# Kernel tuning notes

Hardware: AMD Instinct MI355X
Metric: run time of the kernel (lower is better)

The kernel has to match this reference:

```python
import jax, jax.numpy as jnp
import numpy as np

# config constants (match init_kwargs)
C = 1024
NH = 16
HS = C // NH
CHUNK = 64          # attn_chunk_size
TOPK = 32           # attn_topk
WINDOW = 4096       # kv_cache_window_size
MIN_KV = 16384      # min_kv_cache_size
MAX_KV = 32768      # max_kv_cache_size
SHORT = 4096        # short_sequence_criteria
CT = 65536          # incoming kv-cache length


def setup_inputs() -> dict:
    key = jax.random.key(0)
    ks = jax.random.split(key, 7)
    s = 1.0 / np.sqrt(C)
    return {
        "x": jax.random.normal(ks[0], (C,), jnp.float32),
        "k_cache": jax.random.normal(ks[1], (1, CT, C), jnp.float32),
        "v_cache": jax.random.normal(ks[2], (1, CT, C), jnp.float32),
        "Wr": jax.random.normal(ks[3], (C, C), jnp.float32) * s,
        "Wk": jax.random.normal(ks[4], (C, C), jnp.float32) * s,
        "Wv": jax.random.normal(ks[5], (C, C), jnp.float32) * s,
        "Wo": jax.random.normal(ks[6], (C, C), jnp.float32) * s,
    }


def _split_heads(t):  # (1, T, C) -> (1, NH, T, HS)
    return t.reshape(1, t.shape[1], NH, HS).transpose(0, 2, 1, 3)


def _update_kv_cache(q, k_cache, v_cache):
    # q: (1,1,C); caches: (1,CT,C). CT > MIN_KV so compression runs.
    past = CT - WINDOW
    kp = _split_heads(k_cache[:, :past])          # (1,NH,past,HS)
    vp = _split_heads(v_cache[:, :past])
    qh = _split_heads(q)                          # (1,NH,1,HS)
    scores = jnp.einsum("bhqd,bhkd->bhqk", qh, kp) / np.sqrt(HS)
    w = jax.nn.softmax(scores, axis=-1)           # (1,NH,1,past)
    vote = w.sum(axis=-2)                         # (1,NH,past)
    keep = MIN_KV - WINDOW                        # per-head tokens kept
    _, idx = jax.lax.top_k(vote, keep)            # (1,NH,keep), descending vote order
    kpc = jnp.take_along_axis(kp, idx[..., None], axis=2)  # (1,NH,keep,HS)
    vpc = jnp.take_along_axis(vp, idx[..., None], axis=2)
    kpc = kpc.transpose(0, 2, 1, 3).reshape(1, keep, C)
    vpc = vpc.transpose(0, 2, 1, 3).reshape(1, keep, C)
    k_new = jnp.concatenate([kpc, k_cache[:, past:]], axis=1)  # (1, MIN_KV, C)
    v_new = jnp.concatenate([vpc, v_cache[:, past:]], axis=1)
    return k_new, v_new


def reference(x, k_cache, v_cache, Wr, Wk, Wv, Wo):
    x2 = x[None, None, :]                         # (1,1,C)
    q = x2 @ Wr.T
    k = x2 @ Wk.T
    v = x2 @ Wv.T

    # CT > MAX_KV -> compress cache (eviction via attention vote per head)
    k_cache, v_cache = _update_kv_cache(q, k_cache, v_cache)
    CT2 = k_cache.shape[1]                        # MIN_KV = 16384 > SHORT -> sparse path

    num_chunks = CT2 // CHUNK
    kc = k_cache.reshape(1, num_chunks, CHUNK, C)
    vc = v_cache.reshape(1, num_chunks, CHUNK, C)
    chunk_key = kc.mean(axis=2)                   # (1,num_chunks,C)
    chunk_score = jnp.einsum("bqc,bkc->bqk", q, chunk_key)
    _, tidx = jax.lax.top_k(chunk_score[0, 0], TOPK)  # (TOPK,)
    topk_k = kc[:, tidx].reshape(1, TOPK * CHUNK, C)
    topk_v = vc[:, tidx].reshape(1, TOPK * CHUNK, C)

    k_comb = jnp.concatenate([topk_k, k], axis=1)  # (1, TOPK*CHUNK+1, C)
    v_comb = jnp.concatenate([topk_v, v], axis=1)

    qh = _split_heads(q)                          # (1,NH,1,HS)
    kh = _split_heads(k_comb)
    vh = _split_heads(v_comb)
    attn = jax.nn.softmax(
        jnp.einsum("bhqd,bhkd->bhqk", qh, kh) / np.sqrt(HS), axis=-1)
    y = jnp.einsum("bhqk,bhkd->bhqd", attn, vh)   # (1,NH,1,HS)
    y = y.transpose(0, 2, 1, 3).reshape(C)
    y = y @ Wo.T
    return y
```

## Files before the change

kernel.cpp:

```cpp
#include <hip/hip_runtime.h>
#include <stdint.h>

#define C      1024
#define NH     16
#define HS     64
#define CT     65536
#define PAST   61440
#define KEEP   12288
#define NCOMP  192
#define NSEL   32
#define NB     8192

__device__ __forceinline__ unsigned int desc_key(float f) {
    unsigned int b = __float_as_uint(f);
    return (b >> 31) ? b : (~b & 0x7FFFFFFFu);
}
__device__ __forceinline__ float u_to_f(unsigned int u) {
    unsigned int b = (u & 0x80000000u) ? u : (0x7FFFFFFFu - u);
    return __uint_as_float(b);
}
__device__ __forceinline__ int bin_of(float s, float hi, float scale) {
    int b = (int)((hi - s) * scale);
    return b < 0 ? 0 : (b > NB - 1 ? NB - 1 : b);
}
__device__ __forceinline__ void load_params(const unsigned* umin, const unsigned* umax,
                                            int h, float* hi, float* sc) {
    float h2 = u_to_f(umin[h]);
    float lo = u_to_f(umax[h]);
    float r = h2 - lo;
    *hi = h2;
    *sc = (r > 0.f) ? (float)(NB - 1) / r : 0.f;
}

__global__ void k_proj(const float* __restrict__ x, const float* __restrict__ Wr,
                       const float* __restrict__ Wk, const float* __restrict__ Wv,
                       float* __restrict__ q, float* __restrict__ kn, float* __restrict__ vn,
                       unsigned* __restrict__ hist, unsigned* __restrict__ umin,
                       unsigned* __restrict__ umax, unsigned long long* __restrict__ cs_fix) {
    int id = blockIdx.x * 256 + threadIdx.x;
    if (id < NH * NB) hist[id] = 0;
    if (blockIdx.x == 700) {
        if (threadIdx.x < 16) umin[threadIdx.x] = 0xFFFFFFFFu;
        else if (threadIdx.x < 32) umax[threadIdx.x - 16] = 0u;
    }
    if (blockIdx.x == 701 && threadIdx.x < 256) cs_fix[threadIdx.x] = 0ull;

    int w = blockIdx.x * (blockDim.x >> 6) + (threadIdx.x >> 6);
    int lane = threadIdx.x & 63;
    int mat = w >> 10, row = w & 1023;
    const float* W = (mat == 0) ? Wr : (mat == 1) ? Wk : Wv;
    const float4* Wrow = (const float4*)(W + (size_t)row * C);
    const float4* x4 = (const float4*)x;
    float acc = 0.f;
#pragma unroll
    for (int i = 0; i < 4; ++i) {
        float4 a = Wrow[i * 64 + lane];
        float4 b = x4[i * 64 + lane];
        acc += a.x * b.x + a.y * b.y + a.z * b.z + a.w * b.w;
    }
#pragma unroll
    for (int off = 32; off; off >>= 1) acc += __shfl_xor(acc, off);
    if (lane == 0) { (mat == 0 ? q : (mat == 1 ? kn : vn))[row] = acc; }
}

__global__ void k_scores(const float* __restrict__ kc, const float* __restrict__ q,
                         float* __restrict__ s, unsigned* __restrict__ umin,
                         unsigned* __restrict__ umax) {
    __shared__ float smn[4][16], smx[4][16];
    int wid = blockIdx.x * (blockDim.x >> 6) + (threadIdx.x >> 6);
    int lane = threadIdx.x & 63, wave = threadIdx.x >> 6;
    int nw = gridDim.x * (blockDim.x >> 6);
    const float4* q4 = (const float4*)q;
    float4 qv[4];
#pragma unroll
    for (int i = 0; i < 4; ++i) qv[i] = q4[i * 64 + lane];
    float mnv[4] = {3.4e38f, 3.4e38f, 3.4e38f, 3.4e38f};
    float mxv[4] = {-3.4e38f, -3.4e38f, -3.4e38f, -3.4e38f};
    for (int t = wid; t < CT; t += nw) {
        const float4* row = (const float4*)(kc + (size_t)t * C);
        float acc[4];
#pragma unroll
        for (int i = 0; i < 4; ++i) {
            float4 a = row[i * 64 + lane];
            acc[i] = a.x * qv[i].x + a.y * qv[i].y + a.z * qv[i].z + a.w * qv[i].w;
        }
#pragma unroll
        for (int off = 8; off; off >>= 1) {
#pragma unroll
            for (int i = 0; i < 4; ++i) acc[i] += __shfl_xor(acc[i], off);
        }
        if ((lane & 15) == 0) {
            int g = lane >> 4;
#pragma unroll
            for (int i = 0; i < 4; ++i) {
                s[(size_t)(4 * i + g) * CT + t] = acc[i];
                if (t < PAST) {
                    mnv[i] = fminf(mnv[i], acc[i]);
                    mxv[i] = fmaxf(mxv[i], acc[i]);
                }
            }
        }
    }
    if ((lane & 15) == 0) {
        int g = lane >> 4;
#pragma unroll
        for (int i = 0; i < 4; ++i) { smn[wave][4 * i + g] = mnv[i]; smx[wave][4 * i + g] = mxv[i]; }
    }
    __syncthreads();
    if (threadIdx.x < 16) {
        int h = threadIdx.x;
        float mn = smn[0][h], mx = smx[0][h];
        for (int w2 = 1; w2 < 4; ++w2) {
            mn = fminf(mn, smn[w2][h]);
            mx = fmaxf(mx, smx[w2][h]);
        }
        atomicMin(&umin[h], desc_key(mx));
        atomicMax(&umax[h], desc_key(mn));
    }
}

__global__ __launch_bounds__(1024) void s1_hist(const float* __restrict__ s,
                                                unsigned* __restrict__ hist,
                                                const unsigned* __restrict__ umin,
                                                const unsigned* __restrict__ umax) {
    __shared__ unsigned lh[NB];
    int h = blockIdx.x >> 2, seg = blockIdx.x & 3;
    int tid = threadIdx.x;
    for (int i = tid; i < NB; i += 1024) lh[i] = 0;
    __syncthreads();
    float hi, sc; load_params(umin, umax, h, &hi, &sc);
    const float* sh = s + (size_t)h * CT + seg * 15360;
    for (int i = tid; i < 15360; i += 1024)
        atomicAdd(&lh[bin_of(sh[i], hi, sc)], 1u);
    __syncthreads();
    unsigned* gh = hist + h * NB;
    for (int i = tid; i < NB; i += 1024) {
        unsigned c = lh[i];
        if (c) atomicAdd(&gh[i], c);
    }
}

__global__ __launch_bounds__(1024) void s2_scan(unsigned* __restrict__ base,
                                                unsigned* __restrict__ Tarr,
                                                const float* __restrict__ s,
                                                unsigned long long* __restrict__ cs_fix) {
    __shared__ unsigned wsum[16];
    int h = blockIdx.x, tid = threadIdx.x, lane = tid & 63, wave = tid >> 6;
    unsigned* B = base + h * NB;
    unsigned cnt[8];
    unsigned loc = 0;
    int b0 = tid * 8;
#pragma unroll
    for (int k = 0; k < 8; ++k) { cnt[k] = B[b0 + k]; loc += cnt[k]; }
    unsigned run = loc;
#pragma unroll
    for (int off = 1; off < 64; off <<= 1) {
        unsigned n = __shfl_up(run, off);
        if (lane >= off) run += n;
    }
    if (lane == 63) wsum[wave] = run;
    __syncthreads();
    if (wave == 0 && lane < 16) {
        unsigned v = wsum[lane];
#pragma unroll
        for (int off = 1; off < 16; off <<= 1) {
            unsigned n = __shfl_up(v, off);
            if (lane >= off) v += n;
        }
        wsum[lane] = v;
    }
    __syncthreads();
    unsigned r = run - loc + (wave ? wsum[wave - 1] : 0u);
#pragma unroll
    for (int k = 0; k < 8; ++k) {
        unsigned c = cnt[k];
        B[b0 + k] = r;
        unsigned inc = r + c;
        if (r < KEEP && inc >= KEEP) Tarr[h] = (unsigned)(b0 + k);
        r = inc;
    }
    const float* sh = s + (size_t)h * CT;
#pragma unroll
    for (int k = 0; k < 4; ++k) {
        int i = tid + k * 1024;
        float v = sh[PAST + i];
        long long f = llrintf(v * 16777216.f);
#pragma unroll
        for (int off = 32; off; off >>= 1) f += __shfl_xor(f, off);
        if (lane == 0) atomicAdd(&cs_fix[NCOMP + k * 16 + wave], (unsigned long long)f);
    }
}

__global__ __launch_bounds__(1024) void s3_scatter(const float* __restrict__ s,
                                                   unsigned* __restrict__ base,
                                                   const unsigned* __restrict__ Tarr,
                                                   unsigned long long* __restrict__ G,
                                                   const unsigned* __restrict__ umin,
                                                   const unsigned* __restrict__ umax) {
    int h = blockIdx.x / 60, seg = blockIdx.x % 60;
    int t = seg * 1024 + threadIdx.x;
    float hi, sc; load_params(umin, umax, h, &hi, &sc);
    float v = s[(size_t)h * CT + t];
    int b = bin_of(v, hi, sc);
    if ((unsigned)b <= Tarr[h]) {
        unsigned pos = atomicAdd(&base[h * NB + b], 1u);
        G[(size_t)h * 65536 + pos] = ((unsigned long long)desc_key(v) << 16) | (unsigned)t;
    }
}

__global__ __launch_bounds__(1024) void s4_rank(const unsigned* __restrict__ base,
                                                const unsigned* __restrict__ Tarr,
                                                const unsigned long long* __restrict__ G,
                                                const unsigned* __restrict__ umin,
                                                const unsigned* __restrict__ umax,
                                                unsigned short* __restrict__ stok,
                                                unsigned long long* __restrict__ cs_fix) {
    __shared__ unsigned long long csl[NCOMP];
    int h = blockIdx.x >> 4, seg = blockIdx.x & 15;
    int tid = threadIdx.x;
    if (tid < NCOMP) csl[tid] = 0ull;
    __syncthreads();
    float hi, sc; load_params(umin, umax, h, &hi, &sc);
    unsigned T = Tarr[h];
    unsigned ncand = base[h * NB + T];
    const unsigned long long* Gh = G + (size_t)h * 65536;
    for (unsigned p = seg * 1024 + tid; p < ncand; p += 16384) {
        unsigned long long pk = Gh[p];
        unsigned u = (unsigned)(pk >> 16);
        float v = u_to_f(u);
        int b = bin_of(v, hi, sc);
        unsigned start = b ? base[h * NB + b - 1] : 0u;
        unsigned end = base[h * NB + b];
        unsigned rank = start;
        for (unsigned j = start; j < end; ++j) rank += (Gh[j] < pk) ? 1u : 0u;
        if (rank < KEEP) {
            stok[h * KEEP + rank] = (unsigned short)(pk & 0xFFFFull);
            long long f = llrintf(v * 16777216.f);
            atomicAdd(&csl[rank >> 6], (unsigned long long)f);
        }
    }
    __syncthreads();
    if (tid < NCOMP && csl[tid]) atomicAdd(&cs_fix[tid], csl[tid]);
}

__global__ void k_top32(const unsigned long long* __restrict__ cs_fix,
                        unsigned int* __restrict__ sel) {
    __shared__ unsigned long long key[256];
    int tid = threadIdx.x;
    long long v = (long long)cs_fix[tid];
    unsigned long long bb = (unsigned long long)(v + (1ll << 45));
    key[tid] = (((1ull << 46) - bb) << 8) | (unsigned)tid;
    __syncthreads();
    for (unsigned k = 2; k <= 256; k <<= 1) {
        for (unsigned j = k >> 1; j > 0; j >>= 1) {
            unsigned ixj = tid ^ j;
            if (ixj > (unsigned)tid) {
                unsigned long long a = key[tid], b = key[ixj];
                bool up = ((tid & k) == 0);
                bool sw = up ? (a > b) : (a < b);
                if (sw) { key[tid] = b; key[ixj] = a; }
            }
            __syncthreads();
        }
    }
    if (tid < NSEL) sel[tid] = (unsigned int)(key[tid] & 0xFFull);
}

__global__ void k_attn_part(const float* __restrict__ s, const float* __restrict__ vc,
                            const unsigned short* __restrict__ stok,
                            const unsigned int* __restrict__ sel,
                            float* __restrict__ part) {
    int h = blockIdx.x >> 5, ci = blockIdx.x & 31;
    int tid = threadIdx.x;
    int g = tid >> 2, b3 = tid & 3;
    int c = (int)sel[ci];
    int t = (c < NCOMP) ? (int)stok[h * KEEP + c * 64 + g]
                        : (PAST + (c - NCOMP) * 64 + g);
    __shared__ float scm[64];
    __shared__ float ex[64];
    __shared__ float vbuf[64][65];
    if (b3 == 0) scm[g] = s[(size_t)h * CT + t] * 0.125f;
    __syncthreads();
    float m = -1e30f;
    for (int j = 0; j < 64; ++j) m = fmaxf(m, scm[j]);
    float e = expf(scm[g] - m);
    const float4* vrow = (const float4*)(vc + (size_t)t * C + h * HS);
#pragma unroll
    for (int it = 0; it < 4; ++it) {
        float4 vv = vrow[it * 4 + b3];
        int d0 = it * 16 + b3 * 4;
        vbuf[g][d0 + 0] = e * vv.x;
        vbuf[g][d0 + 1] = e * vv.y;
        vbuf[g][d0 + 2] = e * vv.z;
        vbuf[g][d0 + 3] = e * vv.w;
    }
    if (b3 == 0) ex[g] = e;
    __syncthreads();
    if (tid < 64) {
        float acc = 0.f;
        for (int g2 = 0; g2 < 64; ++g2) acc += vbuf[g2][tid];
        float* P = part + (size_t)(h * 32 + ci) * 68;
        P[2 + tid] = acc;
        if (tid == 0) {
            float es = 0.f;
            for (int g2 = 0; g2 < 64; ++g2) es += ex[g2];
            P[0] = m;
            P[1] = es;
        }
    }
}

__global__ void k_attn_fin(const float* __restrict__ part, const float* __restrict__ q,
                           const float* __restrict__ kn, const float* __restrict__ vn,
                           float* __restrict__ y) {
    int h = blockIdx.x;
    int lane = threadIdx.x;
    float qd = q[h * HS + lane] * kn[h * HS + lane];
#pragma unroll
    for (int off = 32; off; off >>= 1) qd += __shfl_xor(qd, off);
    float a_new = qd * 0.125f;
    const float* P0 = part + (size_t)h * 32 * 68;
    float m = a_new;
    for (int ci = 0; ci < 32; ++ci) m = fmaxf(m, P0[ci * 68]);
    float den = expf(a_new - m);
    float acc = den * vn[h * HS + lane];
    for (int ci = 0; ci < 32; ++ci) {
        float w = expf(P0[ci * 68] - m);
        den += w * P0[ci * 68 + 1];
        acc += w * P0[ci * 68 + 2 + lane];
    }
    y[h * HS + lane] = acc / den;
}

__global__ void k_out(const float* __restrict__ Wo, const float* __restrict__ y,
                      float* __restrict__ out) {
    int w = blockIdx.x * (blockDim.x >> 6) + (threadIdx.x >> 6);
    int lane = threadIdx.x & 63;
    const float4* Wrow = (const float4*)(Wo + (size_t)w * C);
    const float4* y4 = (const float4*)y;
    float acc = 0.f;
#pragma unroll
    for (int i = 0; i < 4; ++i) {
        float4 a = Wrow[i * 64 + lane];
        float4 b = y4[i * 64 + lane];
        acc += a.x * b.x + a.y * b.y + a.z * b.z + a.w * b.w;
    }
#pragma unroll
    for (int off = 32; off; off >>= 1) acc += __shfl_xor(acc, off);
    if (lane == 0) out[w] = acc;
}

extern "C" void kernel_launch(void* const* d_in, const int* in_sizes, int n_in,
                              void* d_out, int out_size, void* d_ws, size_t ws_size,
                              hipStream_t stream) {
    const float* x  = (const float*)d_in[0];
    const float* kc = (const float*)d_in[1];
    const float* vc = (const float*)d_in[2];
    const float* Wr = (const float*)d_in[3];
    const float* Wk = (const float*)d_in[4];
    const float* Wv = (const float*)d_in[5];
    const float* Wo = (const float*)d_in[6];
    float* out = (float*)d_out;
    char* ws = (char*)d_ws;

    float* q    = (float*)(ws + 0);
    float* kn   = (float*)(ws + 8192);
    float* vn   = (float*)(ws + 16384);
    float* y    = (float*)(ws + 24576);
    unsigned long long* cs_fix = (unsigned long long*)(ws + 32768);
    unsigned int* sel = (unsigned int*)(ws + 40960);
    float* part = (float*)(ws + 49152);
    unsigned short* stok = (unsigned short*)(ws + 196608);
    unsigned* umin = (unsigned*)(ws + 602112);
    unsigned* umax = (unsigned*)(ws + 602176);
    unsigned* Tarr = (unsigned*)(ws + 602240);
    unsigned* base = (unsigned*)(ws + 655360);
    float* s = (float*)(ws + 2097152);
    unsigned long long* G = (unsigned long long*)(ws + 6291456);

    k_proj<<<768, 256, 0, stream>>>(x, Wr, Wk, Wv, q, kn, vn, base, umin, umax, cs_fix);
    k_scores<<<2048, 256, 0, stream>>>(kc, q, s, umin, umax);
    s1_hist<<<64, 1024, 0, stream>>>(s, base, umin, umax);
    s2_scan<<<16, 1024, 0, stream>>>(base, Tarr, s, cs_fix);
    s3_scatter<<<960, 1024, 0, stream>>>(s, base, Tarr, G, umin, umax);
    s4_rank<<<256, 1024, 0, stream>>>(base, Tarr, G, umin, umax, stok, cs_fix);
    k_top32<<<1, 256, 0, stream>>>(cs_fix, sel);
    k_attn_part<<<512, 256, 0, stream>>>(s, vc, stok, sel, part);
    k_attn_fin<<<16, 64, 0, stream>>>(part, q, kn, vn, y);
    k_out<<<256, 256, 0, stream>>>(Wo, y, out);
}
```

Before: 142.8 us.

## Fuse post-score pipeline into persistent kernel with software grid barriers

Merges the histogram, scan, scatter, rank, top-32 selection, partial attention, attention finalisation and output projection kernels into one persistent 256-block kernel. Stages are separated by atomic-counter grid barriers instead of separate launches. The score kernel also gives each wave a contiguous 16-token tile and stages results through shared memory for coalesced writes, with min/max taken only over past blocks. The aim is to remove the launch gaps between many small dependent kernels. In exchange it depends on all 256 blocks being co-resident to avoid deadlock, and the top-32 sort is redundantly recomputed in every block.

Measured after the change: 225.2 us. +57.6%, slower.

```diff
diff --git a/kernel.cpp b/kernel.cpp
--- a/kernel.cpp
+++ b/kernel.cpp
@@ -10,6 +10,9 @@
 #define NCOMP  192
 #define NSEL   32
 #define NB     8192
+#define NBLK   256
+
+typedef unsigned long long ull;
 
 __device__ __forceinline__ unsigned int desc_key(float f) {
     unsigned int b = __float_as_uint(f);
@@ -32,13 +35,26 @@
     *sc = (r > 0.f) ? (float)(NB - 1) / r : 0.f;
 }
 
+__device__ __forceinline__ void gsync(unsigned* cnt) {
+    __syncthreads();
+    if (threadIdx.x == 0) {
+        __threadfence();
+        atomicAdd(cnt, 1u);
+        while (atomicAdd(cnt, 0u) < NBLK) __builtin_amdgcn_s_sleep(8);
+        __threadfence();
+    }
+    __syncthreads();
+}
+
 __global__ void k_proj(const float* __restrict__ x, const float* __restrict__ Wr,
                        const float* __restrict__ Wk, const float* __restrict__ Wv,
                        float* __restrict__ q, float* __restrict__ kn, float* __restrict__ vn,
                        unsigned* __restrict__ hist, unsigned* __restrict__ umin,
-                       unsigned* __restrict__ umax, unsigned long long* __restrict__ cs_fix) {
+                       unsigned* __restrict__ umax, ull* __restrict__ cs_fix,
+                       unsigned* __restrict__ bar) {
     int id = blockIdx.x * 256 + threadIdx.x;
     if (id < NH * NB) hist[id] = 0;
+    if (blockIdx.x == 699 && threadIdx.x < 8) bar[threadIdx.x] = 0u;
     if (blockIdx.x == 700) {
         if (threadIdx.x < 16) umin[threadIdx.x] = 0xFFFFFFFFu;
         else if (threadIdx.x < 32) umax[threadIdx.x - 16] = 0u;
@@ -66,18 +82,19 @@
 __global__ void k_scores(const float* __restrict__ kc, const float* __restrict__ q,
                          float* __restrict__ s, unsigned* __restrict__ umin,
                          unsigned* __restrict__ umax) {
+    __shared__ float sc_l[4][16][17];
     __shared__ float smn[4][16], smx[4][16];
-    int wid = blockIdx.x * (blockDim.x >> 6) + (threadIdx.x >> 6);
-    int lane = threadIdx.x & 63, wave = threadIdx.x >> 6;
-    int nw = gridDim.x * (blockDim.x >> 6);
+    int wave = threadIdx.x >> 6, lane = threadIdx.x & 63;
+    int wid = blockIdx.x * 4 + wave;
+    int t0 = wid * 16;
     const float4* q4 = (const float4*)q;
     float4 qv[4];
 #pragma unroll
     for (int i = 0; i < 4; ++i) qv[i] = q4[i * 64 + lane];
     float mnv[4] = {3.4e38f, 3.4e38f, 3.4e38f, 3.4e38f};
     float mxv[4] = {-3.4e38f, -3.4e38f, -3.4e38f, -3.4e38f};
-    for (int t = wid; t < CT; t += nw) {
-        const float4* row = (const float4*)(kc + (size_t)t * C);
+    for (int tt = 0; tt < 16; ++tt) {
+        const float4* row = (const float4*)(kc + (size_t)(t0 + tt) * C);
         float acc[4];
 #pragma unroll
         for (int i = 0; i < 4; ++i) {
@@ -93,261 +110,265 @@
             int g = lane >> 4;
 #pragma unroll
             for (int i = 0; i < 4; ++i) {
-                s[(size_t)(4 * i + g) * CT + t] = acc[i];
-                if (t < PAST) {
-                    mnv[i] = fminf(mnv[i], acc[i]);
-                    mxv[i] = fmaxf(mxv[i], acc[i]);
+                sc_l[wave][4 * i + g][tt] = acc[i];
+                mnv[i] = fminf(mnv[i], acc[i]);
+                mxv[i] = fmaxf(mxv[i], acc[i]);
+            }
+        }
+    }
+    __syncthreads();
+    int tt2 = lane & 15;
+#pragma unroll
+    for (int r = 0; r < 4; ++r) {
+        int h = r * 4 + (lane >> 4);
+        s[(size_t)h * CT + t0 + tt2] = sc_l[wave][h][tt2];
+    }
+    if (blockIdx.x < 960) {
+        if ((lane & 15) == 0) {
+            int g = lane >> 4;
+#pragma unroll
+            for (int i = 0; i < 4; ++i) { smn[wave][4 * i + g] = mnv[i]; smx[wave][4 * i + g] = mxv[i]; }
+        }
+        __syncthreads();
+        if (threadIdx.x < 16) {
+            int h = threadIdx.x;
+            float mn = smn[0][h], mx = smx[0][h];
+            for (int w2 = 1; w2 < 4; ++w2) {
+                mn = fminf(mn, smn[w2][h]);
+                mx = fmaxf(mx, smx[w2][h]);
+            }
+            atomicMin(&umin[h], desc_key(mx));
+            atomicMax(&umax[h], desc_key(mn));
+        }
+    }
+}
+
+__global__ __launch_bounds__(1024, 4) void k_mega(
+        const float* __restrict__ s, const float* __restrict__ vc,
+        const unsigned* __restrict__ umin, const unsigned* __restrict__ umax,
+        unsigned* __restrict__ base, unsigned* __restrict__ Tarr,
+        ull* __restrict__ G, unsigned short* __restrict__ stok,
+        ull* __restrict__ cs_fix, float* __restrict__ part,
+        const float* __restrict__ q, const float* __restrict__ kn,
+        const float* __restrict__ vn, const float* __restrict__ Wo,
+        float* __restrict__ out, unsigned* __restrict__ bar) {
+    const int bid = blockIdx.x, tid = threadIdx.x;
+    const int lane = tid & 63, wave = tid >> 6;
+    __shared__ __align__(16) char smem[40960];
+
+    {
+        unsigned* lh = (unsigned*)smem;
+        int h = bid >> 4, seg = bid & 15;
+        for (int i = tid; i < NB; i += 1024) lh[i] = 0;
+        __syncthreads();
+        float hi, sc; load_params(umin, umax, h, &hi, &sc);
+        const float* sh = s + (size_t)h * CT + seg * 3840;
+        for (int i = tid; i < 3840; i += 1024)
+            atomicAdd(&lh[bin_of(sh[i], hi, sc)], 1u);
+        __syncthreads();
+        unsigned* gh = base + h * NB;
+        for (int i = tid; i < NB; i += 1024) {
+            unsigned c = lh[i];
+            if (c) atomicAdd(&gh[i], c);
+        }
+    }
+    gsync(bar + 0);
+
+    if (bid < 16) {
+        unsigned* wsum = (unsigned*)smem;
+        int h = bid;
+        unsigned* B = base + h * NB;
+        unsigned cnt[8];
+        unsigned loc = 0;
+        int b0 = tid * 8;
+#pragma unroll
+        for (int k = 0; k < 8; ++k) { cnt[k] = B[b0 + k]; loc += cnt[k]; }
+        unsigned run = loc;
+#pragma unroll
+        for (int off = 1; off < 64; off <<= 1) {
+            unsigned n = __shfl_up(run, off);
+            if (lane >= off) run += n;
+        }
+        if (lane == 63) wsum[wave] = run;
+        __syncthreads();
+        if (wave == 0 && lane < 16) {
+            unsigned v = wsum[lane];
+#pragma unroll
+            for (int off = 1; off < 16; off <<= 1) {
+                unsigned n = __shfl_up(v, off);
+                if (lane >= off) v += n;
+            }
+            wsum[lane] = v;
+        }
+        __syncthreads();
+        unsigned r = run - loc + (wave ? wsum[wave - 1] : 0u);
+#pragma unroll
+        for (int k = 0; k < 8; ++k) {
+            unsigned c = cnt[k];
+            B[b0 + k] = r;
+            unsigned inc = r + c;
+            if (r < KEEP && inc >= KEEP) Tarr[h] = (unsigned)(b0 + k);
+            r = inc;
+        }
+    } else {
+        int gw = (bid - 16) * 16 + wave;
+        if (gw < NH * 64) {
+            int h = gw >> 6, c2 = gw & 63;
+            float v = s[(size_t)h * CT + PAST + c2 * 64 + lane];
+            long long f = llrintf(v * 16777216.f);
+#pragma unroll
+            for (int off = 32; off; off >>= 1) f += __shfl_xor(f, off);
+            if (lane == 0) atomicAdd(&cs_fix[NCOMP + c2], (ull)f);
+        }
+    }
+    gsync(bar + 1);
+
+    for (int i = bid * 1024 + tid; i < NH * PAST; i += NBLK * 1024) {
+        int h = i / PAST, t = i - h * PAST;
+        float hi, sc; load_params(umin, umax, h, &hi, &sc);
+        float v = s[(size_t)h * CT + t];
+        int b = bin_of(v, hi, sc);
+        if ((unsigned)b <= Tarr[h]) {
+            unsigned pos = atomicAdd(&base[h * NB + b], 1u);
+            G[(size_t)h * 65536 + pos] = ((ull)desc_key(v) << 16) | (unsigned)t;
+        }
+    }
+    gsync(bar + 2);
+
+    {
+        ull* csl = (ull*)smem;
+        if (tid < NCOMP) csl[tid] = 0ull;
+        __syncthreads();
+        int h = bid >> 4, seg = bid & 15;
+        float hi, sc; load_params(umin, umax, h, &hi, &sc);
+        unsigned T = Tarr[h];
+        unsigned ncand = base[h * NB + T];
+        const ull* Gh = G + (size_t)h * 65536;
+        for (unsigned p = seg * 1024 + tid; p < ncand; p += 16384) {
+            ull pk = Gh[p];
+            unsigned u = (unsigned)(pk >> 16);
+            float v = u_to_f(u);
+            int b = bin_of(v, hi, sc);
+            unsigned start = b ? base[h * NB + b - 1] : 0u;
+            unsigned end = base[h * NB + b];
+            unsigned rank = start;
+            for (unsigned j = start; j < end; ++j) rank += (Gh[j] < pk) ? 1u : 0u;
+            if (rank < KEEP) {
+                stok[h * KEEP + rank] = (unsigned short)(pk & 0xFFFFull);
+                long long f = llrintf(v * 16777216.f);
+                atomicAdd(&csl[rank >> 6], (ull)f);
+            }
+        }
+        __syncthreads();
+        if (tid < NCOMP) {
+            ull c = csl[tid];
+            if (c) atomicAdd(&cs_fix[tid], c);
+        }
+    }
+    gsync(bar + 3);
+
+    {
+        ull* key = (ull*)smem;
+        unsigned* sel_l = (unsigned*)(smem + 2048);
+        float* scm = (float*)(smem + 2176);
+        float* exb = (float*)(smem + 2688);
+        float* vbuf = (float*)(smem + 3200);
+        if (tid < 256) {
+            long long v = (long long)cs_fix[tid];
+            ull bb = (ull)(v + (1ll << 45));
+            key[tid] = (((1ull << 46) - bb) << 8) | (unsigned)tid;
+        }
+        __syncthreads();
+        for (unsigned k = 2; k <= 256; k <<= 1) {
+            for (unsigned j = k >> 1; j > 0; j >>= 1) {
+                if (tid < 256) {
+                    unsigned ixj = tid ^ j;
+                    if (ixj > (unsigned)tid) {
+                        ull a = key[tid], b = key[ixj];
+                        bool up = ((tid & k) == 0);
+                        if (up ? (a > b) : (a < b)) { key[tid] = b; key[ixj] = a; }
+                    }
                 }
-            }
-        }
-    }
-    if ((lane & 15) == 0) {
-        int g = lane >> 4;
-#pragma unroll
-        for (int i = 0; i < 4; ++i) { smn[wave][4 * i + g] = mnv[i]; smx[wave][4 * i + g] = mxv[i]; }
-    }
-    __syncthreads();
-    if (threadIdx.x < 16) {
-        int h = threadIdx.x;
-        float mn = smn[0][h], mx = smx[0][h];
-        for (int w2 = 1; w2 < 4; ++w2) {
-            mn = fminf(mn, smn[w2][h]);
-            mx = fmaxf(mx, smx[w2][h]);
-        }
-        atomicMin(&umin[h], desc_key(mx));
-        atomicMax(&umax[h], desc_key(mn));
-    }
-}
-
-__global__ __launch_bounds__(1024) void s1_hist(const float* __restrict__ s,
-                                                unsigned* __restrict__ hist,
-                                                const unsigned* __restrict__ umin,
-                                                const unsigned* __restrict__ umax) {
-    __shared__ unsigned lh[NB];
-    int h = blockIdx.x >> 2, seg = blockIdx.x & 3;
-    int tid = threadIdx.x;
-    for (int i = tid; i < NB; i += 1024) lh[i] = 0;
-    __syncthreads();
-    float hi, sc; load_params(umin, umax, h, &hi, &sc);
-    const float* sh = s + (size_t)h * CT + seg * 15360;
-    for (int i = tid; i < 15360; i += 1024)
-        atomicAdd(&lh[bin_of(sh[i], hi, sc)], 1u);
-    __syncthreads();
-    unsigned* gh = hist + h * NB;
-    for (int i = tid; i < NB; i += 1024) {
-        unsigned c = lh[i];
-        if (c) atomicAdd(&gh[i], c);
-    }
-}
-
-__global__ __launch_bounds__(1024) void s2_scan(unsigned* __restrict__ base,
-                                                unsigned* __restrict__ Tarr,
-                                                const float* __restrict__ s,
-                                                unsigned long long* __restrict__ cs_fix) {
-    __shared__ unsigned wsum[16];
-    int h = blockIdx.x, tid = threadIdx.x, lane = tid & 63, wave = tid >> 6;
-    unsigned* B = base + h * NB;
-    unsigned cnt[8];
-    unsigned loc = 0;
-    int b0 = tid * 8;
-#pragma unroll
-    for (int k = 0; k < 8; ++k) { cnt[k] = B[b0 + k]; loc += cnt[k]; }
-    unsigned run = loc;
-#pragma unroll
-    for (int off = 1; off < 64; off <<= 1) {
-        unsigned n = __shfl_up(run, off);
-        if (lane >= off) run += n;
-    }
-    if (lane == 63) wsum[wave] = run;
-    __syncthreads();
-    if (wave == 0 && lane < 16) {
-        unsigned v = wsum[lane];
-#pragma unroll
-        for (int off = 1; off < 16; off <<= 1) {
-            unsigned n = __shfl_up(v, off);
-            if (lane >= off) v += n;
-        }
-        wsum[lane] = v;
-    }
-    __syncthreads();
-    unsigned r = run - loc + (wave ? wsum[wave - 1] : 0u);
-#pragma unroll
-    for (int k = 0; k < 8; ++k) {
-        unsigned c = cnt[k];
-        B[b0 + k] = r;
-        unsigned inc = r + c;
-        if (r < KEEP && inc >= KEEP) Tarr[h] = (unsigned)(b0 + k);
-        r = inc;
-    }
-    const float* sh = s + (size_t)h * CT;
-#pragma unroll
-    for (int k = 0; k < 4; ++k) {
-        int i = tid + k * 1024;
-        float v = sh[PAST + i];
-        long long f = llrintf(v * 16777216.f);
-#pragma unroll
-        for (int off = 32; off; off >>= 1) f += __shfl_xor(f, off);
-        if (lane == 0) atomicAdd(&cs_fix[NCOMP + k * 16 + wave], (unsigned long long)f);
-    }
-}
-
-__global__ __launch_bounds__(1024) void s3_scatter(const float* __restrict__ s,
-                                                   unsigned* __restrict__ base,
-                                                   const unsigned* __restrict__ Tarr,
-                                                   unsigned long long* __restrict__ G,
-                                                   const unsigned* __restrict__ umin,
-                                                   const unsigned* __restrict__ umax) {
-    int h = blockIdx.x / 60, seg = blockIdx.x % 60;
-    int t = seg * 1024 + threadIdx.x;
-    float hi, sc; load_params(umin, umax, h, &hi, &sc);
-    float v = s[(size_t)h * CT + t];
-    int b = bin_of(v, hi, sc);
-    if ((unsigned)b <= Tarr[h]) {
-        unsigned pos = atomicAdd(&base[h * NB + b], 1u);
-        G[(size_t)h * 65536 + pos] = ((unsigned long long)desc_key(v) << 16) | (unsigned)t;
-    }
-}
-
-__global__ __launch_bounds__(1024) void s4_rank(const unsigned* __restrict__ base,
-                                                const unsigned* __restrict__ Tarr,
-                                                const unsigned long long* __restrict__ G,
-                                                const unsigned* __restrict__ umin,
-                                                const unsigned* __restrict__ umax,
-                                                unsigned short* __restrict__ stok,
-                                                unsigned long long* __restrict__ cs_fix) {
-    __shared__ unsigned long long csl[NCOMP];
-    int h = blockIdx.x >> 4, seg = blockIdx.x & 15;
-    int tid = threadIdx.x;
-    if (tid < NCOMP) csl[tid] = 0ull;
-    __syncthreads();
-    float hi, sc; load_params(umin, umax, h, &hi, &sc);
-    unsigned T = Tarr[h];
-    unsigned ncand = base[h * NB + T];
-    const unsigned long long* Gh = G + (size_t)h * 65536;
-    for (unsigned p = seg * 1024 + tid; p < ncand; p += 16384) {
-        unsigned long long pk = Gh[p];
-        unsigned u = (unsigned)(pk >> 16);
-        float v = u_to_f(u);
-        int b = bin_of(v, hi, sc);
-        unsigned start = b ? base[h * NB + b - 1] : 0u;
-        unsigned end = base[h * NB + b];
-        unsigned rank = start;
-        for (unsigned j = start; j < end; ++j) rank += (Gh[j] < pk) ? 1u : 0u;
-        if (rank < KEEP) {
-            stok[h * KEEP + rank] = (unsigned short)(pk & 0xFFFFull);
-            long long f = llrintf(v * 16777216.f);
-            atomicAdd(&csl[rank >> 6], (unsigned long long)f);
-        }
-    }
-    __syncthreads();
-    if (tid < NCOMP && csl[tid]) atomicAdd(&cs_fix[tid], csl[tid]);
-}
-
-__global__ void k_top32(const unsigned long long* __restrict__ cs_fix,
-                        unsigned int* __restrict__ sel) {
-    __shared__ unsigned long long key[256];
-    int tid = threadIdx.x;
-    long long v = (long long)cs_fix[tid];
-    unsigned long long bb = (unsigned long long)(v + (1ll << 45));
-    key[tid] = (((1ull << 46) - bb) << 8) | (unsigned)tid;
-    __syncthreads();
-    for (unsigned k = 2; k <= 256; k <<= 1) {
-        for (unsigned j = k >> 1; j > 0; j >>= 1) {
-            unsigned ixj = tid ^ j;
-            if (ixj > (unsigned)tid) {
-                unsigned long long a = key[tid], b = key[ixj];
-                bool up = ((tid & k) == 0);
-                bool sw = up ? (a > b) : (a < b);
-                if (sw) { key[tid] = b; key[ixj] = a; }
-            }
-            __syncthreads();
-        }
-    }
-    if (tid < NSEL) sel[tid] = (unsigned int)(key[tid] & 0xFFull);
-}
-
-__global__ void k_attn_part(const float* __restrict__ s, const float* __restrict__ vc,
-                            const unsigned short* __restrict__ stok,
-                            const unsigned int* __restrict__ sel,
-                            float* __restrict__ part) {
-    int h = blockIdx.x >> 5, ci = blockIdx.x & 31;
-    int tid = threadIdx.x;
-    int g = tid >> 2, b3 = tid & 3;
-    int c = (int)sel[ci];
-    int t = (c < NCOMP) ? (int)stok[h * KEEP + c * 64 + g]
-                        : (PAST + (c - NCOMP) * 64 + g);
-    __shared__ float scm[64];
-    __shared__ float ex[64];
-    __shared__ float vbuf[64][65];
-    if (b3 == 0) scm[g] = s[(size_t)h * CT + t] * 0.125f;
-    __syncthreads();
-    float m = -1e30f;
-    for (int j = 0; j < 64; ++j) m = fmaxf(m, scm[j]);
-    float e = expf(scm[g] - m);
-    const float4* vrow = (const float4*)(vc + (size_t)t * C + h * HS);
-#pragma unroll
-    for (int it = 0; it < 4; ++it) {
-        float4 vv = vrow[it * 4 + b3];
-        int d0 = it * 16 + b3 * 4;
-        vbuf[g][d0 + 0] = e * vv.x;
-        vbuf[g][d0 + 1] = e * vv.y;
-        vbuf[g][d0 + 2] = e * vv.z;
-        vbuf[g][d0 + 3] = e * vv.w;
-    }
-    if (b3 == 0) ex[g] = e;
-    __syncthreads();
-    if (tid < 64) {
+                __syncthreads();
+            }
+        }
+        if (tid < NSEL) sel_l[tid] = (unsigned)(key[tid] & 0xFFull);
+        __syncthreads();
+
+        int su = tid >> 9, sid = tid & 511;
+        int p = bid * 2 + su;
+        int h = p >> 5, ci = p & 31;
+        int c = (int)sel_l[ci];
+        int g = sid >> 3, q8 = sid & 7;
+        int t = (c < NCOMP) ? (int)stok[h * KEEP + c * 64 + g]
+                            : (PAST + (c - NCOMP) * 64 + g);
+        if (q8 == 0) scm[su * 64 + g] = s[(size_t)h * CT + t] * 0.125f;
+        __syncthreads();
+        float m = -1e30f;
+        for (int j = 0; j < 64; ++j) m = fmaxf(m, scm[su * 64 + j]);
+        float e = expf(scm[su * 64 + g] - m);
+        if (q8 == 0) exb[su * 64 + g] = e;
+        const float4* vrow = (const float4*)(vc + (size_t)t * C + h * HS);
+        float4 v0 = vrow[q8 * 2], v1 = vrow[q8 * 2 + 1];
+        float* vb = vbuf + su * 4352 + g * 68 + q8 * 8;
+        vb[0] = e * v0.x; vb[1] = e * v0.y; vb[2] = e * v0.z; vb[3] = e * v0.w;
+        vb[4] = e * v1.x; vb[5] = e * v1.y; vb[6] = e * v1.z; vb[7] = e * v1.w;
+        __syncthreads();
+        if (sid < 64) {
+            float acc = 0.f;
+            for (int g2 = 0; g2 < 64; ++g2) acc += vbuf[su * 4352 + g2 * 68 + sid];
+            float* P = part + (size_t)(h * 32 + ci) * 68;
+            P[2 + sid] = acc;
+            if (sid == 0) {
+                float es = 0.f;
+                for (int g2 = 0; g2 < 64; ++g2) es += exb[su * 64 + g2];
+                P[0] = m;
+                P[1] = es;
+            }
+        }
+    }
+    gsync(bar + 4);
+    if (bid >= 64) return;
+
+    {
+        float* yl = (float*)smem;
+        float* qdl = (float*)(smem + 4096);
+        if (tid < 16) {
+            float qd = 0.f;
+            for (int l = 0; l < 64; ++l) qd += q[tid * 64 + l] * kn[tid * 64 + l];
+            qdl[tid] = qd;
+        }
+        __syncthreads();
+        {
+            int h = tid >> 6, ln = tid & 63;
+            float a_new = qdl[h] * 0.125f;
+            const float* P0 = part + (size_t)h * 32 * 68;
+            float m = a_new;
+            for (int ci = 0; ci < 32; ++ci) m = fmaxf(m, P0[ci * 68]);
+            float den = expf(a_new - m);
+            float acc = den * vn[h * HS + ln];
+            for (int ci = 0; ci < 32; ++ci) {
+                float w = expf(P0[ci * 68] - m);
+                den += w * P0[ci * 68 + 1];
+                acc += w * P0[ci * 68 + 2 + ln];
+            }
+            yl[tid] = acc / den;
+        }
+        __syncthreads();
+        int r = bid * 16 + wave;
+        const float4* Wrow = (const float4*)(Wo + (size_t)r * C);
+        const float4* y4 = (const float4*)yl;
         float acc = 0.f;
-        for (int g2 = 0; g2 < 64; ++g2) acc += vbuf[g2][tid];
-        float* P = part + (size_t)(h * 32 + ci) * 68;
-        P[2 + tid] = acc;
-        if (tid == 0) {
-            float es = 0.f;
-            for (int g2 = 0; g2 < 64; ++g2) es += ex[g2];
-            P[0] = m;
-            P[1] = es;
-        }
-    }
-}
-
-__global__ void k_attn_fin(const float* __restrict__ part, const float* __restrict__ q,
-                           const float* __restrict__ kn, const float* __restrict__ vn,
-                           float* __restrict__ y) {
-    int h = blockIdx.x;
-    int lane = threadIdx.x;
-    float qd = q[h * HS + lane] * kn[h * HS + lane];
-#pragma unroll
-    for (int off = 32; off; off >>= 1) qd += __shfl_xor(qd, off);
-    float a_new = qd * 0.125f;
-    const float* P0 = part + (size_t)h * 32 * 68;
-    float m = a_new;
-    for (int ci = 0; ci < 32; ++ci) m = fmaxf(m, P0[ci * 68]);
-    float den = expf(a_new - m);
-    float acc = den * vn[h * HS + lane];
-    for (int ci = 0; ci < 32; ++ci) {
-        float w = expf(P0[ci * 68] - m);
-        den += w * P0[ci * 68 + 1];
-        acc += w * P0[ci * 68 + 2 + lane];
-    }
-    y[h * HS + lane] = acc / den;
-}
-
-__global__ void k_out(const float* __restrict__ Wo, const float* __restrict__ y,
-                      float* __restrict__ out) {
-    int w = blockIdx.x * (blockDim.x >> 6) + (threadIdx.x >> 6);
-    int lane = threadIdx.x & 63;
-    const float4* Wrow = (const float4*)(Wo + (size_t)w * C);
-    const float4* y4 = (const float4*)y;
-    float acc = 0.f;
-#pragma unroll
-    for (int i = 0; i < 4; ++i) {
-        float4 a = Wrow[i * 64 + lane];
-        float4 b = y4[i * 64 + lane];
-        acc += a.x * b.x + a.y * b.y + a.z * b.z + a.w * b.w;
-    }
-#pragma unroll
-    for (int off = 32; off; off >>= 1) acc += __shfl_xor(acc, off);
-    if (lane == 0) out[w] = acc;
+#pragma unroll
+        for (int i = 0; i < 4; ++i) {
+            float4 a = Wrow[i * 64 + lane];
+            float4 b = y4[i * 64 + lane];
+            acc += a.x * b.x + a.y * b.y + a.z * b.z + a.w * b.w;
+        }
+#pragma unroll
+        for (int off = 32; off; off >>= 1) acc += __shfl_xor(acc, off);
+        if (lane == 0) out[r] = acc;
+    }
 }
 
 extern "C" void kernel_launch(void* const* d_in, const int* in_sizes, int n_in,
@@ -366,26 +387,19 @@
     float* q    = (float*)(ws + 0);
     float* kn   = (float*)(ws + 8192);
     float* vn   = (float*)(ws + 16384);
-    float* y    = (float*)(ws + 24576);
-    unsigned long long* cs_fix = (unsigned long long*)(ws + 32768);
-    unsigned int* sel = (unsigned int*)(ws + 40960);
+    ull* cs_fix = (ull*)(ws + 32768);
     float* part = (float*)(ws + 49152);
     unsigned short* stok = (unsigned short*)(ws + 196608);
     unsigned* umin = (unsigned*)(ws + 602112);
     unsigned* umax = (unsigned*)(ws + 602176);
     unsigned* Tarr = (unsigned*)(ws + 602240);
+    unsigned* bar  = (unsigned*)(ws + 602368);
     unsigned* base = (unsigned*)(ws + 655360);
     float* s = (float*)(ws + 2097152);
-    unsigned long long* G = (unsigned long long*)(ws + 6291456);
-
-    k_proj<<<768, 256, 0, stream>>>(x, Wr, Wk, Wv, q, kn, vn, base, umin, umax, cs_fix);
-    k_scores<<<2048, 256, 0, stream>>>(kc, q, s, umin, umax);
-    s1_hist<<<64, 1024, 0, stream>>>(s, base, umin, umax);
-    s2_scan<<<16, 1024, 0, stream>>>(base, Tarr, s, cs_fix);
-    s3_scatter<<<960, 1024, 0, stream>>>(s, base, Tarr, G, umin, umax);
-    s4_rank<<<256, 1024, 0, stream>>>(base, Tarr, G, umin, umax, stok, cs_fix);
-    k_top32<<<1, 256, 0, stream>>>(cs_fix, sel);
-    k_attn_part<<<512, 256, 0, stream>>>(s, vc, stok, sel, part);
-    k_attn_fin<<<16, 64, 0, stream>>>(part, q, kn, vn, y);
-    k_out<<<256, 256, 0, stream>>>(Wo, y, out);
-}
+    ull* G = (ull*)(ws + 6291456);
+
+    k_proj<<<768, 256, 0, stream>>>(x, Wr, Wk, Wv, q, kn, vn, base, umin, umax, cs_fix, bar);
+    k_scores<<<1024, 256, 0, stream>>>(kc, q, s, umin, umax);
+    k_mega<<<NBLK, 1024, 0, stream>>>(s, vc, umin, umax, base, Tarr, G, stok, cs_fix,
+                                      part, q, kn, vn, Wo, out, bar);
+}
```

## Fuse pipeline stages with last-block barriers to cut kernel launches

Applied to the files above, without the earlier changes.

Merges several small kernels. The histogram scan moves into the last-arriving block of s1_hist, the top-32 chunk sort into the last block of s4_rank, and attention finalize plus output projection into one kernel that recomputes y per block. k_scores now processes contiguous 64-token tiles staged in shared memory, so score stores are coalesced, and the window-chunk sum moves into it. This removes three launches and their gaps in exchange for atomic counters, fences, a serial per-lane scan in one block, and redundant finalize work in each of the 64 output blocks.

Measured after the change: 457.3 us. 3.2x slower.

```diff
diff --git a/kernel.cpp b/kernel.cpp
--- a/kernel.cpp
+++ b/kernel.cpp
@@ -11,6 +11,8 @@
 #define NSEL   32
 #define NB     8192
 
+typedef unsigned long long ull;
+
 __device__ __forceinline__ unsigned int desc_key(float f) {
     unsigned int b = __float_as_uint(f);
     return (b >> 31) ? b : (~b & 0x7FFFFFFFu);
@@ -36,9 +38,11 @@
                        const float* __restrict__ Wk, const float* __restrict__ Wv,
                        float* __restrict__ q, float* __restrict__ kn, float* __restrict__ vn,
                        unsigned* __restrict__ hist, unsigned* __restrict__ umin,
-                       unsigned* __restrict__ umax, unsigned long long* __restrict__ cs_fix) {
+                       unsigned* __restrict__ umax, ull* __restrict__ cs_fix,
+                       unsigned* __restrict__ bar) {
     int id = blockIdx.x * 256 + threadIdx.x;
     if (id < NH * NB) hist[id] = 0;
+    if (blockIdx.x == 699 && threadIdx.x < 8) bar[threadIdx.x] = 0u;
     if (blockIdx.x == 700) {
         if (threadIdx.x < 16) umin[threadIdx.x] = 0xFFFFFFFFu;
         else if (threadIdx.x < 32) umax[threadIdx.x - 16] = 0u;
@@ -63,21 +67,21 @@
     if (lane == 0) { (mat == 0 ? q : (mat == 1 ? kn : vn))[row] = acc; }
 }
 
-__global__ void k_scores(const float* __restrict__ kc, const float* __restrict__ q,
-                         float* __restrict__ s, unsigned* __restrict__ umin,
-                         unsigned* __restrict__ umax) {
-    __shared__ float smn[4][16], smx[4][16];
-    int wid = blockIdx.x * (blockDim.x >> 6) + (threadIdx.x >> 6);
-    int lane = threadIdx.x & 63, wave = threadIdx.x >> 6;
-    int nw = gridDim.x * (blockDim.x >> 6);
+__global__ __launch_bounds__(512) void k_scores(const float* __restrict__ kc,
+                         const float* __restrict__ q, float* __restrict__ s,
+                         unsigned* __restrict__ umin, unsigned* __restrict__ umax,
+                         ull* __restrict__ cs_fix) {
+    __shared__ float sc_l[8][16][8];
+    const int tid = threadIdx.x;
+    const int wave = tid >> 6, lane = tid & 63;
+    const int T0 = blockIdx.x * 64;
+    const int t0 = T0 + wave * 8;
     const float4* q4 = (const float4*)q;
     float4 qv[4];
 #pragma unroll
     for (int i = 0; i < 4; ++i) qv[i] = q4[i * 64 + lane];
-    float mnv[4] = {3.4e38f, 3.4e38f, 3.4e38f, 3.4e38f};
-    float mxv[4] = {-3.4e38f, -3.4e38f, -3.4e38f, -3.4e38f};
-    for (int t = wid; t < CT; t += nw) {
-        const float4* row = (const float4*)(kc + (size_t)t * C);
+    for (int tt = 0; tt < 8; ++tt) {
+        const float4* row = (const float4*)(kc + (size_t)(t0 + tt) * C);
         float acc[4];
 #pragma unroll
         for (int i = 0; i < 4; ++i) {
@@ -92,109 +96,91 @@
         if ((lane & 15) == 0) {
             int g = lane >> 4;
 #pragma unroll
-            for (int i = 0; i < 4; ++i) {
-                s[(size_t)(4 * i + g) * CT + t] = acc[i];
-                if (t < PAST) {
-                    mnv[i] = fminf(mnv[i], acc[i]);
-                    mxv[i] = fmaxf(mxv[i], acc[i]);
-                }
-            }
-        }
-    }
-    if ((lane & 15) == 0) {
-        int g = lane >> 4;
-#pragma unroll
-        for (int i = 0; i < 4; ++i) { smn[wave][4 * i + g] = mnv[i]; smx[wave][4 * i + g] = mxv[i]; }
-    }
-    __syncthreads();
-    if (threadIdx.x < 16) {
-        int h = threadIdx.x;
-        float mn = smn[0][h], mx = smx[0][h];
-        for (int w2 = 1; w2 < 4; ++w2) {
-            mn = fminf(mn, smn[w2][h]);
-            mx = fmaxf(mx, smx[w2][h]);
-        }
-        atomicMin(&umin[h], desc_key(mx));
-        atomicMax(&umax[h], desc_key(mn));
+            for (int i = 0; i < 4; ++i) sc_l[wave][4 * i + g][tt] = acc[i];
+        }
+    }
+    __syncthreads();
+    const int h = tid >> 5, toff = (tid & 31) * 2;
+    float v0 = sc_l[toff >> 3][h][toff & 7];
+    float v1 = sc_l[toff >> 3][h][(toff & 7) + 1];
+    s[(size_t)h * CT + T0 + toff] = v0;
+    s[(size_t)h * CT + T0 + toff + 1] = v1;
+    if (blockIdx.x < 960) {
+        float mn = fminf(v0, v1), mx = fmaxf(v0, v1);
+#pragma unroll
+        for (int off = 16; off; off >>= 1) {
+            mn = fminf(mn, __shfl_xor(mn, off));
+            mx = fmaxf(mx, __shfl_xor(mx, off));
+        }
+        if ((tid & 31) == 0) {
+            atomicMin(&umin[h], desc_key(mx));
+            atomicMax(&umax[h], desc_key(mn));
+        }
+    } else {
+        long long f = llrintf(v0 * 16777216.f) + llrintf(v1 * 16777216.f);
+#pragma unroll
+        for (int off = 16; off; off >>= 1) f += __shfl_xor(f, off);
+        if ((tid & 31) == 0)
+            atomicAdd(&cs_fix[NCOMP + (blockIdx.x - 960)], (ull)f);
     }
 }
 
 __global__ __launch_bounds__(1024) void s1_hist(const float* __restrict__ s,
-                                                unsigned* __restrict__ hist,
+                                                unsigned* __restrict__ base,
                                                 const unsigned* __restrict__ umin,
-                                                const unsigned* __restrict__ umax) {
+                                                const unsigned* __restrict__ umax,
+                                                unsigned* __restrict__ Tarr,
+                                                unsigned* __restrict__ bar) {
     __shared__ unsigned lh[NB];
-    int h = blockIdx.x >> 2, seg = blockIdx.x & 3;
-    int tid = threadIdx.x;
-    for (int i = tid; i < NB; i += 1024) lh[i] = 0;
-    __syncthreads();
-    float hi, sc; load_params(umin, umax, h, &hi, &sc);
-    const float* sh = s + (size_t)h * CT + seg * 15360;
-    for (int i = tid; i < 15360; i += 1024)
-        atomicAdd(&lh[bin_of(sh[i], hi, sc)], 1u);
-    __syncthreads();
-    unsigned* gh = hist + h * NB;
-    for (int i = tid; i < NB; i += 1024) {
-        unsigned c = lh[i];
-        if (c) atomicAdd(&gh[i], c);
-    }
-}
-
-__global__ __launch_bounds__(1024) void s2_scan(unsigned* __restrict__ base,
-                                                unsigned* __restrict__ Tarr,
-                                                const float* __restrict__ s,
-                                                unsigned long long* __restrict__ cs_fix) {
-    __shared__ unsigned wsum[16];
-    int h = blockIdx.x, tid = threadIdx.x, lane = tid & 63, wave = tid >> 6;
-    unsigned* B = base + h * NB;
-    unsigned cnt[8];
-    unsigned loc = 0;
-    int b0 = tid * 8;
-#pragma unroll
-    for (int k = 0; k < 8; ++k) { cnt[k] = B[b0 + k]; loc += cnt[k]; }
-    unsigned run = loc;
-#pragma unroll
-    for (int off = 1; off < 64; off <<= 1) {
-        unsigned n = __shfl_up(run, off);
-        if (lane >= off) run += n;
-    }
-    if (lane == 63) wsum[wave] = run;
-    __syncthreads();
-    if (wave == 0 && lane < 16) {
-        unsigned v = wsum[lane];
-#pragma unroll
-        for (int off = 1; off < 16; off <<= 1) {
-            unsigned n = __shfl_up(v, off);
-            if (lane >= off) v += n;
-        }
-        wsum[lane] = v;
-    }
-    __syncthreads();
-    unsigned r = run - loc + (wave ? wsum[wave - 1] : 0u);
-#pragma unroll
-    for (int k = 0; k < 8; ++k) {
-        unsigned c = cnt[k];
-        B[b0 + k] = r;
-        unsigned inc = r + c;
-        if (r < KEEP && inc >= KEEP) Tarr[h] = (unsigned)(b0 + k);
-        r = inc;
-    }
-    const float* sh = s + (size_t)h * CT;
-#pragma unroll
-    for (int k = 0; k < 4; ++k) {
-        int i = tid + k * 1024;
-        float v = sh[PAST + i];
-        long long f = llrintf(v * 16777216.f);
-#pragma unroll
-        for (int off = 32; off; off >>= 1) f += __shfl_xor(f, off);
-        if (lane == 0) atomicAdd(&cs_fix[NCOMP + k * 16 + wave], (unsigned long long)f);
+    __shared__ unsigned sh_last;
+    const int tid = threadIdx.x;
+    const int lane = tid & 63, wave = tid >> 6;
+    {
+        int h = blockIdx.x >> 2, seg = blockIdx.x & 3;
+        for (int i = tid; i < NB; i += 1024) lh[i] = 0;
+        __syncthreads();
+        float hi, sc; load_params(umin, umax, h, &hi, &sc);
+        const float* sh = s + (size_t)h * CT + seg * 15360;
+        for (int i = tid; i < 15360; i += 1024)
+            atomicAdd(&lh[bin_of(sh[i], hi, sc)], 1u);
+        __syncthreads();
+        unsigned* gh = base + h * NB;
+        for (int i = tid; i < NB; i += 1024) {
+            unsigned c = lh[i];
+            if (c) atomicAdd(&gh[i], c);
+        }
+    }
+    __threadfence();
+    if (tid == 0) sh_last = (atomicAdd(&bar[0], 1u) == 63u) ? 1u : 0u;
+    __syncthreads();
+    if (!sh_last) return;
+    __threadfence();
+    {
+        unsigned* B = base + wave * NB;
+        int b0 = lane * 128;
+        unsigned lsum = 0;
+        for (int k = 0; k < 128; ++k) lsum += B[b0 + k];
+        unsigned run = lsum;
+#pragma unroll
+        for (int off = 1; off < 64; off <<= 1) {
+            unsigned n = __shfl_up(run, off);
+            if (lane >= off) run += n;
+        }
+        unsigned r = run - lsum;
+        for (int k = 0; k < 128; ++k) {
+            unsigned c = B[b0 + k];
+            B[b0 + k] = r;
+            unsigned inc = r + c;
+            if (r < KEEP && inc >= KEEP) Tarr[wave] = (unsigned)(b0 + k);
+            r = inc;
+        }
     }
 }
 
 __global__ __launch_bounds__(1024) void s3_scatter(const float* __restrict__ s,
                                                    unsigned* __restrict__ base,
                                                    const unsigned* __restrict__ Tarr,
-                                                   unsigned long long* __restrict__ G,
+                                                   ull* __restrict__ G,
                                                    const unsigned* __restrict__ umin,
                                                    const unsigned* __restrict__ umax) {
     int h = blockIdx.x / 60, seg = blockIdx.x % 60;
@@ -204,66 +190,77 @@
     int b = bin_of(v, hi, sc);
     if ((unsigned)b <= Tarr[h]) {
         unsigned pos = atomicAdd(&base[h * NB + b], 1u);
-        G[(size_t)h * 65536 + pos] = ((unsigned long long)desc_key(v) << 16) | (unsigned)t;
+        G[(size_t)h * 65536 + pos] = ((ull)desc_key(v) << 16) | (unsigned)t;
     }
 }
 
 __global__ __launch_bounds__(1024) void s4_rank(const unsigned* __restrict__ base,
                                                 const unsigned* __restrict__ Tarr,
-                                                const unsigned long long* __restrict__ G,
+                                                const ull* __restrict__ G,
                                                 const unsigned* __restrict__ umin,
                                                 const unsigned* __restrict__ umax,
                                                 unsigned short* __restrict__ stok,
-                                                unsigned long long* __restrict__ cs_fix) {
-    __shared__ unsigned long long csl[NCOMP];
-    int h = blockIdx.x >> 4, seg = blockIdx.x & 15;
-    int tid = threadIdx.x;
-    if (tid < NCOMP) csl[tid] = 0ull;
-    __syncthreads();
-    float hi, sc; load_params(umin, umax, h, &hi, &sc);
-    unsigned T = Tarr[h];
-    unsigned ncand = base[h * NB + T];
-    const unsigned long long* Gh = G + (size_t)h * 65536;
-    for (unsigned p = seg * 1024 + tid; p < ncand; p += 16384) {
-        unsigned long long pk = Gh[p];
-        unsigned u = (unsigned)(pk >> 16);
-        float v = u_to_f(u);
-        int b = bin_of(v, hi, sc);
-        unsigned start = b ? base[h * NB + b - 1] : 0u;
-        unsigned end = base[h * NB + b];
-        unsigned rank = start;
-        for (unsigned j = start; j < end; ++j) rank += (Gh[j] < pk) ? 1u : 0u;
-        if (rank < KEEP) {
-            stok[h * KEEP + rank] = (unsigned short)(pk & 0xFFFFull);
-            long long f = llrintf(v * 16777216.f);
-            atomicAdd(&csl[rank >> 6], (unsigned long long)f);
-        }
-    }
-    __syncthreads();
-    if (tid < NCOMP && csl[tid]) atomicAdd(&cs_fix[tid], csl[tid]);
-}
-
-__global__ void k_top32(const unsigned long long* __restrict__ cs_fix,
-                        unsigned int* __restrict__ sel) {
-    __shared__ unsigned long long key[256];
-    int tid = threadIdx.x;
-    long long v = (long long)cs_fix[tid];
-    unsigned long long bb = (unsigned long long)(v + (1ll << 45));
-    key[tid] = (((1ull << 46) - bb) << 8) | (unsigned)tid;
+                                                ull* __restrict__ cs_fix,
+                                                unsigned* __restrict__ sel,
+                                                unsigned* __restrict__ bar) {
+    __shared__ ull csl[NCOMP];
+    __shared__ unsigned sh_last;
+    __shared__ ull key[256];
+    const int tid = threadIdx.x;
+    {
+        if (tid < NCOMP) csl[tid] = 0ull;
+        __syncthreads();
+        int h = blockIdx.x >> 4, seg = blockIdx.x & 15;
+        float hi, sc; load_params(umin, umax, h, &hi, &sc);
+        unsigned T = Tarr[h];
+        unsigned ncand = base[h * NB + T];
+        const ull* Gh = G + (size_t)h * 65536;
+        for (unsigned p = seg * 1024 + tid; p < ncand; p += 16384) {
+            ull pk = Gh[p];
+            unsigned u = (unsigned)(pk >> 16);
+            float v = u_to_f(u);
+            int b = bin_of(v, hi, sc);
+            unsigned start = b ? base[h * NB + b - 1] : 0u;
+            unsigned end = base[h * NB + b];
+            unsigned rank = start;
+            for (unsigned j = start; j < end; ++j) rank += (Gh[j] < pk) ? 1u : 0u;
+            if (rank < KEEP) {
+                stok[h * KEEP + rank] = (unsigned short)(pk & 0xFFFFull);
+                long long f = llrintf(v * 16777216.f);
+                atomicAdd(&csl[rank >> 6], (ull)f);
+            }
+        }
+        __syncthreads();
+        if (tid < NCOMP) {
+            ull c = csl[tid];
+            if (c) atomicAdd(&cs_fix[tid], c);
+        }
+    }
+    __threadfence();
+    if (tid == 0) sh_last = (atomicAdd(&bar[1], 1u) == 255u) ? 1u : 0u;
+    __syncthreads();
+    if (!sh_last) return;
+    __threadfence();
+    if (tid < 256) {
+        long long v = (long long)cs_fix[tid];
+        ull bb = (ull)(v + (1ll << 45));
+        key[tid] = (((1ull << 46) - bb) << 8) | (unsigned)tid;
+    }
     __syncthreads();
     for (unsigned k = 2; k <= 256; k <<= 1) {
         for (unsigned j = k >> 1; j > 0; j >>= 1) {
-            unsigned ixj = tid ^ j;
-            if (ixj > (unsigned)tid) {
-                unsigned long long a = key[tid], b = key[ixj];
-                bool up = ((tid & k) == 0);
-                bool sw = up ? (a > b) : (a < b);
-                if (sw) { key[tid] = b; key[ixj] = a; }
+            if (tid < 256) {
+                unsigned ixj = tid ^ j;
+                if (ixj > (unsigned)tid) {
+                    ull a = key[tid], b = key[ixj];
+                    bool up = ((tid & k) == 0);
+                    if (up ? (a > b) : (a < b)) { key[tid] = b; key[ixj] = a; }
+                }
             }
             __syncthreads();
         }
     }
-    if (tid < NSEL) sel[tid] = (unsigned int)(key[tid] & 0xFFull);
+    if (tid < NSEL) sel[tid] = (unsigned)(key[tid] & 0xFFull);
 }
 
 __global__ void k_attn_part(const float* __restrict__ s, const float* __restrict__ vc,
@@ -310,34 +307,38 @@
     }
 }
 
-__global__ void k_attn_fin(const float* __restrict__ part, const float* __restrict__ q,
-                           const float* __restrict__ kn, const float* __restrict__ vn,
-                           float* __restrict__ y) {
-    int h = blockIdx.x;
-    int lane = threadIdx.x;
-    float qd = q[h * HS + lane] * kn[h * HS + lane];
-#pragma unroll
-    for (int off = 32; off; off >>= 1) qd += __shfl_xor(qd, off);
-    float a_new = qd * 0.125f;
-    const float* P0 = part + (size_t)h * 32 * 68;
-    float m = a_new;
-    for (int ci = 0; ci < 32; ++ci) m = fmaxf(m, P0[ci * 68]);
-    float den = expf(a_new - m);
-    float acc = den * vn[h * HS + lane];
-    for (int ci = 0; ci < 32; ++ci) {
-        float w = expf(P0[ci * 68] - m);
-        den += w * P0[ci * 68 + 1];
-        acc += w * P0[ci * 68 + 2 + lane];
-    }
-    y[h * HS + lane] = acc / den;
-}
-
-__global__ void k_out(const float* __restrict__ Wo, const float* __restrict__ y,
-                      float* __restrict__ out) {
-    int w = blockIdx.x * (blockDim.x >> 6) + (threadIdx.x >> 6);
-    int lane = threadIdx.x & 63;
-    const float4* Wrow = (const float4*)(Wo + (size_t)w * C);
-    const float4* y4 = (const float4*)y;
+__global__ __launch_bounds__(1024) void k_finout(const float* __restrict__ part,
+        const float* __restrict__ q, const float* __restrict__ kn,
+        const float* __restrict__ vn, const float* __restrict__ Wo,
+        float* __restrict__ out) {
+    __shared__ float yl[1024];
+    __shared__ float qdl[16];
+    const int tid = threadIdx.x, wave = tid >> 6, lane = tid & 63;
+    {
+        float p = q[wave * 64 + lane] * kn[wave * 64 + lane];
+#pragma unroll
+        for (int off = 32; off; off >>= 1) p += __shfl_xor(p, off);
+        if (lane == 0) qdl[wave] = p;
+    }
+    __syncthreads();
+    {
+        float a_new = qdl[wave] * 0.125f;
+        const float* P0 = part + (size_t)wave * 32 * 68;
+        float m = a_new;
+        for (int ci = 0; ci < 32; ++ci) m = fmaxf(m, P0[ci * 68]);
+        float den = expf(a_new - m);
+        float acc = den * vn[wave * HS + lane];
+        for (int ci = 0; ci < 32; ++ci) {
+            float w = expf(P0[ci * 68] - m);
+            den += w * P0[ci * 68 + 1];
+            acc += w * P0[ci * 68 + 2 + lane];
+        }
+        yl[tid] = acc / den;
+    }
+    __syncthreads();
+    int r = blockIdx.x * 16 + wave;
+    const float4* Wrow = (const float4*)(Wo + (size_t)r * C);
+    const float4* y4 = (const float4*)yl;
     float acc = 0.f;
 #pragma unroll
     for (int i = 0; i < 4; ++i) {
@@ -347,7 +348,7 @@
     }
 #pragma unroll
     for (int off = 32; off; off >>= 1) acc += __shfl_xor(acc, off);
-    if (lane == 0) out[w] = acc;
+    if (lane == 0) out[r] = acc;
 }
 
 extern "C" void kernel_launch(void* const* d_in, const int* in_sizes, int n_in,
@@ -366,26 +367,23 @@
     float* q    = (float*)(ws + 0);
     float* kn   = (float*)(ws + 8192);
     float* vn   = (float*)(ws + 16384);
-    float* y    = (float*)(ws + 24576);
-    unsigned long long* cs_fix = (unsigned long long*)(ws + 32768);
-    unsigned int* sel = (unsigned int*)(ws + 40960);
+    ull* cs_fix = (ull*)(ws + 32768);
+    unsigned* sel = (unsigned*)(ws + 40960);
     float* part = (float*)(ws + 49152);
     unsigned short* stok = (unsigned short*)(ws + 196608);
     unsigned* umin = (unsigned*)(ws + 602112);
     unsigned* umax = (unsigned*)(ws + 602176);
     unsigned* Tarr = (unsigned*)(ws + 602240);
+    unsigned* bar  = (unsigned*)(ws + 602368);
     unsigned* base = (unsigned*)(ws + 655360);
     float* s = (float*)(ws + 2097152);
-    unsigned long long* G = (unsigned long long*)(ws + 6291456);
-
-    k_proj<<<768, 256, 0, stream>>>(x, Wr, Wk, Wv, q, kn, vn, base, umin, umax, cs_fix);
-    k_scores<<<2048, 256, 0, stream>>>(kc, q, s, umin, umax);
-    s1_hist<<<64, 1024, 0, stream>>>(s, base, umin, umax);
-    s2_scan<<<16, 1024, 0, stream>>>(base, Tarr, s, cs_fix);
+    ull* G = (ull*)(ws + 6291456);
+
+    k_proj<<<768, 256, 0, stream>>>(x, Wr, Wk, Wv, q, kn, vn, base, umin, umax, cs_fix, bar);
+    k_scores<<<1024, 512, 0, stream>>>(kc, q, s, umin, umax, cs_fix);
+    s1_hist<<<64, 1024, 0, stream>>>(s, base, umin, umax, Tarr, bar);
     s3_scatter<<<960, 1024, 0, stream>>>(s, base, Tarr, G, umin, umax);
-    s4_rank<<<256, 1024, 0, stream>>>(base, Tarr, G, umin, umax, stok, cs_fix);
-    k_top32<<<1, 256, 0, stream>>>(cs_fix, sel);
+    s4_rank<<<256, 1024, 0, stream>>>(base, Tarr, G, umin, umax, stok, cs_fix, sel, bar);
     k_attn_part<<<512, 256, 0, stream>>>(s, vc, stok, sel, part);
-    k_attn_fin<<<16, 64, 0, stream>>>(part, q, kn, vn, y);
-    k_out<<<256, 256, 0, stream>>>(Wo, y, out);
-}
+    k_finout<<<64, 1024, 0, stream>>>(part, q, kn, vn, Wo, out);
+}
```
